# Kernel optimization log

Hardware: AMD Instinct MI355X
Metric: run time of the kernel (lower is better)

Reference implementation:

```python
import jax, jax.numpy as jnp
import numpy as np

KERNEL_MUL = 2.0
KERNEL_NUM = 5


def _mmd(source, target):
    n_s = source.shape[0]
    total = jnp.concatenate([source, target], axis=0)  # (2N, D)
    n = total.shape[0]
    # pairwise squared L2 via a^2 + b^2 - 2ab (avoids (2N,2N,D) intermediate)
    sq = jnp.sum(total * total, axis=1)  # (2N,)
    L2 = sq[:, None] + sq[None, :] - 2.0 * (total @ total.T)  # (2N, 2N)
    # torch uses L2_distance.data for bandwidth -> stop_gradient
    bandwidth = jax.lax.stop_gradient(jnp.sum(L2)) / (n * n - n)
    bandwidth = bandwidth / (KERNEL_MUL ** (KERNEL_NUM // 2))
    # multi-bandwidth RBF sum
    kernels = jnp.zeros_like(L2)
    for i in range(KERNEL_NUM):
        kernels = kernels + jnp.exp(-L2 / (bandwidth * KERNEL_MUL ** i))
    XX = kernels[:n_s, :n_s]
    YY = kernels[n_s:, n_s:]
    XY = kernels[:n_s, n_s:]
    YX = kernels[n_s:, :n_s]
    return jnp.mean(XX) + jnp.mean(YY) - jnp.mean(XY) - jnp.mean(YX)


def setup_inputs() -> dict:
    key = jax.random.key(0)
    k1, k2 = jax.random.split(key)
    source = jax.random.normal(k1, (4096, 256), dtype=jnp.float32)
    target = jax.random.normal(k2, (4096, 256), dtype=jnp.float32) + 0.5
    return {"source": source, "target": target}


def reference(source, target):
    return _mmd(source, target)
```

## Files before the change

### kernel.cpp

```cpp
#include <hip/hip_runtime.h>

typedef short bf16x8 __attribute__((ext_vector_type(8)));
typedef float f32x4 __attribute__((ext_vector_type(4)));

#define KDIM 256
#define BT 128
#define SBLK 256


__device__ __forceinline__ unsigned short f2bf(float f) {
  unsigned u = __float_as_uint(f);
  unsigned r = (u + 0x7fffu + ((u >> 16) & 1u)) >> 16;
  return (unsigned short)r;
}
__device__ __forceinline__ float bf2f(unsigned short b) {
  return __uint_as_float(((unsigned)b) << 16);
}

__device__ __forceinline__ float2 pk_add(float2 a, float2 b) {
  return make_float2(a.x + b.x, a.y + b.y);
}
__device__ __forceinline__ float2 pk_mul(float2 a, float2 b) {
  return make_float2(a.x * b.x, a.y * b.y);
}
__device__ __forceinline__ float2 pk_fma(float2 a, float2 b, float2 c) {
  return make_float2(__builtin_fmaf(a.x, b.x, c.x),
                     __builtin_fmaf(a.y, b.y, c.y));
}

__global__ __launch_bounds__(256) void mmd_stage(
    const float* __restrict__ src, const float* __restrict__ tgt, int ns,
    unsigned short* __restrict__ Tp, float* __restrict__ sq,
    float* __restrict__ pscol, float* __restrict__ psums) {
  __shared__ float sp[256];
  __shared__ float rw[4];
  int t = threadIdx.x;
  int lane = t & 63, wave = t >> 6;
  sp[t] = 0.f;
  __syncthreads();
  int sub = t & 31;
  int rsel = t >> 5;
  int ks = sub >> 2, kq = sub & 3;
  float colacc[8];
#pragma unroll
  for (int j = 0; j < 8; ++j) colacc[j] = 0.f;
  float tsq = 0.f;
#pragma unroll
  for (int it = 0; it < 4; ++it) {
    int r = blockIdx.x * 32 + it * 8 + rsel;
    const float* rp = (r < ns) ? (src + (size_t)r * KDIM)
                               : (tgt + (size_t)(r - ns) * KDIM);
    float4 v0 = *(const float4*)(rp + sub * 8);
    float4 v1 = *(const float4*)(rp + sub * 8 + 4);
    float vals[8] = {v0.x, v0.y, v0.z, v0.w, v1.x, v1.y, v1.z, v1.w};
    unsigned pk[4];
    float ssp = 0.f;
#pragma unroll
    for (int j = 0; j < 4; ++j) {
      unsigned short b0 = f2bf(vals[2 * j]);
      unsigned short b1 = f2bf(vals[2 * j + 1]);
      float x0 = bf2f(b0), x1 = bf2f(b1);
      pk[j] = (unsigned)b0 | ((unsigned)b1 << 16);
      ssp += x0 * x0 + x1 * x1;
      colacc[2 * j] += x0;
      colacc[2 * j + 1] += x1;
    }
    size_t poff = (size_t)(r >> 4) * 4096 + ks * 512 + kq * 128 + (r & 15) * 8;
    *(uint4*)(Tp + poff) = make_uint4(pk[0], pk[1], pk[2], pk[3]);
    tsq += ssp;
    float ss = ssp;
#pragma unroll
    for (int off = 16; off; off >>= 1) ss += __shfl_down(ss, off, 32);
    if (sub == 0) sq[r] = ss;
  }
#pragma unroll
  for (int j = 0; j < 8; ++j) atomicAdd(&sp[sub * 8 + j], colacc[j]);
#pragma unroll
  for (int off = 32; off; off >>= 1) tsq += __shfl_down(tsq, off, 64);
  if (lane == 0) rw[wave] = tsq;
  __syncthreads();
  pscol[(size_t)blockIdx.x * 256 + t] = sp[t];
  if (t == 0) psums[blockIdx.x] = rw[0] + rw[1] + rw[2] + rw[3];
}

__global__ __launch_bounds__(256) void mmd_prep2(
    const float* __restrict__ pscol, const float* __restrict__ psums,
    float* __restrict__ coef, float* __restrict__ out, int n) {
  __shared__ float redP[4], redS[4];
  int t = threadIdx.x;
  int lane = t & 63, wave = t >> 6;
  float cs = 0.f;
#pragma unroll 8
  for (int b = 0; b < SBLK; ++b) cs += pscol[(size_t)b * 256 + t];
  float p = cs * cs;
  float s = psums[t];
#pragma unroll
  for (int off = 32; off; off >>= 1) {
    p += __shfl_down(p, off, 64);
    s += __shfl_down(s, off, 64);
  }
  if (lane == 0) { redP[wave] = p; redS[wave] = s; }
  __syncthreads();
  if (t == 0) {
    double ssq = (double)(redP[0] + redP[1] + redP[2] + redP[3]);
    double S = (double)(redS[0] + redS[1] + redS[2] + redS[3]);
    double nn = (double)n;
    double sumL2 = 2.0 * nn * S - 2.0 * ssq;
    double bw = sumL2 / (nn * nn - nn) / 4.0;
    coef[0] = (float)(-1.4426950408889634 / (16.0 * bw));
    out[0] = 0.f;
  }
}

__global__ __launch_bounds__(256) void mmd_main(
    const unsigned short* __restrict__ Tp, const float* __restrict__ sq,
    const float* __restrict__ coef, float* __restrict__ out, int halfTiles,
    float inv) {
  __shared__ float sqa[BT];
  __shared__ float sqb[BT];
  __shared__ float red[4];

  int id = blockIdx.x;
  int bi = (int)((sqrtf(8.f * (float)id + 1.f) - 1.f) * 0.5f);
  while ((bi + 1) * (bi + 2) / 2 <= id) ++bi;
  while (bi * (bi + 1) / 2 > id) --bi;
  int bj = id - bi * (bi + 1) / 2;
  int rowBase = bi * BT, colBase = bj * BT;

  int t = threadIdx.x;
  int lane = t & 63, wave = t >> 6;

  if (t < 128) sqa[t] = sq[rowBase + t];
  else sqb[t - 128] = sq[colBase + (t - 128)];
  __syncthreads();

  int wrow = (wave >> 1) * 64, wcol = (wave & 1) * 64;

  const unsigned short* aB[4];
  const unsigned short* bB[4];
#pragma unroll
  for (int mt = 0; mt < 4; ++mt)
    aB[mt] = Tp + (size_t)(bi * 8 + (wrow >> 4) + mt) * 4096 + lane * 8;
#pragma unroll
  for (int nt = 0; nt < 4; ++nt)
    bB[nt] = Tp + (size_t)(bj * 8 + (wcol >> 4) + nt) * 4096 + lane * 8;

  f32x4 acc[4][4];
#pragma unroll
  for (int a = 0; a < 4; ++a)
#pragma unroll
    for (int b = 0; b < 4; ++b) {
      f32x4 z = {0.f, 0.f, 0.f, 0.f};
      acc[a][b] = z;
    }

#pragma unroll
  for (int ks = 0; ks < 8; ++ks) {
    bf16x8 af[4], bfv[4];
#pragma unroll
    for (int mt = 0; mt < 4; ++mt)
      af[mt] = *(const bf16x8*)(aB[mt] + ks * 512);
#pragma unroll
    for (int nt = 0; nt < 4; ++nt)
      bfv[nt] = *(const bf16x8*)(bB[nt] + ks * 512);
#pragma unroll
    for (int mt = 0; mt < 4; ++mt)
#pragma unroll
      for (int nt = 0; nt < 4; ++nt)
        acc[mt][nt] = __builtin_amdgcn_mfma_f32_16x16x32_bf16(
            af[mt], bfv[nt], acc[mt][nt], 0, 0, 0);
  }

  float c4 = coef[0];
  float m2c4 = -2.f * c4;
  float2 m2v = make_float2(m2c4, m2c4);
  int ccol = lane & 15;
  int rb = (lane >> 4) * 4;
  float ra[16];
#pragma unroll
  for (int mt = 0; mt < 4; ++mt)
#pragma unroll
    for (int rg = 0; rg < 4; ++rg)
      ra[mt * 4 + rg] = sqa[wrow + mt * 16 + rb + rg] * c4;
  float cbv[4];
#pragma unroll
  for (int nt = 0; nt < 4; ++nt) cbv[nt] = sqb[wcol + nt * 16 + ccol] * c4;

  float2 lsum2 = make_float2(0.f, 0.f);
#pragma unroll
  for (int mt = 0; mt < 4; ++mt) {
#pragma unroll
    for (int nt = 0; nt < 4; ++nt) {
      float cb = cbv[nt];
#pragma unroll
      for (int rp = 0; rp < 4; rp += 2) {
        float2 g = make_float2(acc[mt][nt][rp], acc[mt][nt][rp + 1]);
        float2 sab =
            make_float2(ra[mt * 4 + rp] + cb, ra[mt * 4 + rp + 1] + cb);
        float2 u = pk_fma(g, m2v, sab);
        float2 e = make_float2(__builtin_amdgcn_exp2f(u.x),
                               __builtin_amdgcn_exp2f(u.y));
        float2 e2 = pk_mul(e, e);
        float2 e4 = pk_mul(e2, e2);
        float2 e8 = pk_mul(e4, e4);
        float2 s = pk_add(e, e2);
        s = pk_add(s, e4);
        s = pk_add(s, e8);
        s = pk_fma(e8, e8, s);
        lsum2 = pk_add(lsum2, s);
      }
    }
  }
  float lsum = lsum2.x + lsum2.y;
#pragma unroll
  for (int off = 32; off; off >>= 1) lsum += __shfl_down(lsum, off, 64);
  if (lane == 0) red[wave] = lsum;
  __syncthreads();
  if (t == 0) {
    float w = ((bi < halfTiles) == (bj < halfTiles)) ? 1.f : -1.f;
    float f = (bi == bj) ? 1.f : 2.f;
    atomicAdd(out, w * f * inv * (red[0] + red[1] + red[2] + red[3]));
  }
}

extern "C" void kernel_launch(void* const* d_in, const int* in_sizes, int n_in,
                              void* d_out, int out_size, void* d_ws,
                              size_t ws_size, hipStream_t stream) {
  const float* src = (const float*)d_in[0];
  const float* tgt = (const float*)d_in[1];
  int ns = in_sizes[0] / KDIM;
  int ntr = in_sizes[1] / KDIM;
  int n = ns + ntr;

  char* ws = (char*)d_ws;
  unsigned short* Tp = (unsigned short*)ws;
  size_t off = (size_t)n * KDIM * sizeof(unsigned short);
  float* sq = (float*)(ws + off);    off += (size_t)n * 4;
  float* pscol = (float*)(ws + off); off += (size_t)SBLK * 256 * 4;
  float* psums = (float*)(ws + off); off += SBLK * 4;
  float* coef = (float*)(ws + off);

  float* out = (float*)d_out;
  int nb = n / BT;
  int nTiles = nb * (nb + 1) / 2;

  mmd_stage<<<SBLK, 256, 0, stream>>>(src, tgt, ns, Tp, sq, pscol, psums);
  mmd_prep2<<<1, 256, 0, stream>>>(pscol, psums, coef, out, n);
  mmd_main<<<nTiles, 256, 0, stream>>>(Tp, sq, coef, out, ns / BT,
                                       1.f / ((float)ns * (float)ns));
}
```

Before: 114.1 us.

## Make main MMD kernel persistent with grid-stride tile loop and register-side reduction

The main kernel now launches a fixed grid of 768 blocks that loop over triangular tiles with a grid stride, instead of one block per tile. Row norms are read straight from global memory into registers rather than staged through shared memory with a barrier, and per-tile weighted sums are accumulated in registers so each block does a single reduction and atomic at the end. This cuts the number of atomics, barriers and block launches, but tile count (2080) over 768 blocks leaves uneven work per block and gives up overlap between independent blocks.

```diff
diff --git a/kernel.cpp b/kernel.cpp
--- a/kernel.cpp
+++ b/kernel.cpp
@@ -6,6 +6,7 @@
 #define KDIM 256
 #define BT 128
 #define SBLK 256
+#define PBLK 768
 
 
 __device__ __forceinline__ unsigned short f2bf(float f) {
@@ -115,112 +116,107 @@
 __global__ __launch_bounds__(256) void mmd_main(
     const unsigned short* __restrict__ Tp, const float* __restrict__ sq,
     const float* __restrict__ coef, float* __restrict__ out, int halfTiles,
-    float inv) {
-  __shared__ float sqa[BT];
-  __shared__ float sqb[BT];
+    float inv, int nTiles) {
   __shared__ float red[4];
-
-  int id = blockIdx.x;
-  int bi = (int)((sqrtf(8.f * (float)id + 1.f) - 1.f) * 0.5f);
-  while ((bi + 1) * (bi + 2) / 2 <= id) ++bi;
-  while (bi * (bi + 1) / 2 > id) --bi;
-  int bj = id - bi * (bi + 1) / 2;
-  int rowBase = bi * BT, colBase = bj * BT;
-
   int t = threadIdx.x;
   int lane = t & 63, wave = t >> 6;
-
-  if (t < 128) sqa[t] = sq[rowBase + t];
-  else sqb[t - 128] = sq[colBase + (t - 128)];
-  __syncthreads();
-
   int wrow = (wave >> 1) * 64, wcol = (wave & 1) * 64;
-
-  const unsigned short* aB[4];
-  const unsigned short* bB[4];
-#pragma unroll
-  for (int mt = 0; mt < 4; ++mt)
-    aB[mt] = Tp + (size_t)(bi * 8 + (wrow >> 4) + mt) * 4096 + lane * 8;
-#pragma unroll
-  for (int nt = 0; nt < 4; ++nt)
-    bB[nt] = Tp + (size_t)(bj * 8 + (wcol >> 4) + nt) * 4096 + lane * 8;
-
-  f32x4 acc[4][4];
-#pragma unroll
-  for (int a = 0; a < 4; ++a)
-#pragma unroll
-    for (int b = 0; b < 4; ++b) {
-      f32x4 z = {0.f, 0.f, 0.f, 0.f};
-      acc[a][b] = z;
-    }
-
-#pragma unroll
-  for (int ks = 0; ks < 8; ++ks) {
-    bf16x8 af[4], bfv[4];
-#pragma unroll
-    for (int mt = 0; mt < 4; ++mt)
-      af[mt] = *(const bf16x8*)(aB[mt] + ks * 512);
-#pragma unroll
-    for (int nt = 0; nt < 4; ++nt)
-      bfv[nt] = *(const bf16x8*)(bB[nt] + ks * 512);
-#pragma unroll
-    for (int mt = 0; mt < 4; ++mt)
-#pragma unroll
-      for (int nt = 0; nt < 4; ++nt)
-        acc[mt][nt] = __builtin_amdgcn_mfma_f32_16x16x32_bf16(
-            af[mt], bfv[nt], acc[mt][nt], 0, 0, 0);
-  }
+  int ccol = lane & 15;
+  int rb = (lane >> 4) * 4;
 
   float c4 = coef[0];
   float m2c4 = -2.f * c4;
   float2 m2v = make_float2(m2c4, m2c4);
-  int ccol = lane & 15;
-  int rb = (lane >> 4) * 4;
-  float ra[16];
-#pragma unroll
-  for (int mt = 0; mt < 4; ++mt)
-#pragma unroll
-    for (int rg = 0; rg < 4; ++rg)
-      ra[mt * 4 + rg] = sqa[wrow + mt * 16 + rb + rg] * c4;
-  float cbv[4];
-#pragma unroll
-  for (int nt = 0; nt < 4; ++nt) cbv[nt] = sqb[wcol + nt * 16 + ccol] * c4;
-
-  float2 lsum2 = make_float2(0.f, 0.f);
-#pragma unroll
-  for (int mt = 0; mt < 4; ++mt) {
-#pragma unroll
-    for (int nt = 0; nt < 4; ++nt) {
-      float cb = cbv[nt];
-#pragma unroll
-      for (int rp = 0; rp < 4; rp += 2) {
-        float2 g = make_float2(acc[mt][nt][rp], acc[mt][nt][rp + 1]);
-        float2 sab =
-            make_float2(ra[mt * 4 + rp] + cb, ra[mt * 4 + rp + 1] + cb);
-        float2 u = pk_fma(g, m2v, sab);
-        float2 e = make_float2(__builtin_amdgcn_exp2f(u.x),
-                               __builtin_amdgcn_exp2f(u.y));
-        float2 e2 = pk_mul(e, e);
-        float2 e4 = pk_mul(e2, e2);
-        float2 e8 = pk_mul(e4, e4);
-        float2 s = pk_add(e, e2);
-        s = pk_add(s, e4);
-        s = pk_add(s, e8);
-        s = pk_fma(e8, e8, s);
-        lsum2 = pk_add(lsum2, s);
+  float wsum = 0.f;
+
+  for (int id = blockIdx.x; id < nTiles; id += gridDim.x) {
+    int bi = (int)((sqrtf(8.f * (float)id + 1.f) - 1.f) * 0.5f);
+    while ((bi + 1) * (bi + 2) / 2 <= id) ++bi;
+    while (bi * (bi + 1) / 2 > id) --bi;
+    int bj = id - bi * (bi + 1) / 2;
+
+    float sra[16];
+#pragma unroll
+    for (int mt = 0; mt < 4; ++mt)
+#pragma unroll
+      for (int rg = 0; rg < 4; ++rg)
+        sra[mt * 4 + rg] = sq[bi * BT + wrow + mt * 16 + rb + rg];
+    float scb[4];
+#pragma unroll
+    for (int nt = 0; nt < 4; ++nt)
+      scb[nt] = sq[bj * BT + wcol + nt * 16 + ccol];
+
+    const unsigned short* aB[4];
+    const unsigned short* bB[4];
+#pragma unroll
+    for (int mt = 0; mt < 4; ++mt)
+      aB[mt] = Tp + (size_t)(bi * 8 + (wrow >> 4) + mt) * 4096 + lane * 8;
+#pragma unroll
+    for (int nt = 0; nt < 4; ++nt)
+      bB[nt] = Tp + (size_t)(bj * 8 + (wcol >> 4) + nt) * 4096 + lane * 8;
+
+    f32x4 acc[4][4];
+#pragma unroll
+    for (int a = 0; a < 4; ++a)
+#pragma unroll
+      for (int b = 0; b < 4; ++b) {
+        f32x4 z = {0.f, 0.f, 0.f, 0.f};
+        acc[a][b] = z;
+      }
+
+#pragma unroll
+    for (int ks = 0; ks < 8; ++ks) {
+      bf16x8 af[4], bfv[4];
+#pragma unroll
+      for (int mt = 0; mt < 4; ++mt)
+        af[mt] = *(const bf16x8*)(aB[mt] + ks * 512);
+#pragma unroll
+      for (int nt = 0; nt < 4; ++nt)
+        bfv[nt] = *(const bf16x8*)(bB[nt] + ks * 512);
+#pragma unroll
+      for (int mt = 0; mt < 4; ++mt)
+#pragma unroll
+        for (int nt = 0; nt < 4; ++nt)
+          acc[mt][nt] = __builtin_amdgcn_mfma_f32_16x16x32_bf16(
+              af[mt], bfv[nt], acc[mt][nt], 0, 0, 0);
+    }
+
+    float2 lsum2 = make_float2(0.f, 0.f);
+#pragma unroll
+    for (int mt = 0; mt < 4; ++mt) {
+#pragma unroll
+      for (int nt = 0; nt < 4; ++nt) {
+        float cb = scb[nt] * c4;
+#pragma unroll
+        for (int rp = 0; rp < 4; rp += 2) {
+          float2 g = make_float2(acc[mt][nt][rp], acc[mt][nt][rp + 1]);
+          float2 sab = make_float2(
+              __builtin_fmaf(sra[mt * 4 + rp], c4, cb),
+              __builtin_fmaf(sra[mt * 4 + rp + 1], c4, cb));
+          float2 u = pk_fma(g, m2v, sab);
+          float2 e = make_float2(__builtin_amdgcn_exp2f(u.x),
+                                 __builtin_amdgcn_exp2f(u.y));
+          float2 e2 = pk_mul(e, e);
+          float2 e4 = pk_mul(e2, e2);
+          float2 e8 = pk_mul(e4, e4);
+          float2 s = pk_add(e, e2);
+          s = pk_add(s, e4);
+          s = pk_add(s, e8);
+          s = pk_fma(e8, e8, s);
+          lsum2 = pk_add(lsum2, s);
+        }
       }
     }
-  }
-  float lsum = lsum2.x + lsum2.y;
-#pragma unroll
-  for (int off = 32; off; off >>= 1) lsum += __shfl_down(lsum, off, 64);
-  if (lane == 0) red[wave] = lsum;
-  __syncthreads();
-  if (t == 0) {
-    float w = ((bi < halfTiles) == (bj < halfTiles)) ? 1.f : -1.f;
-    float f = (bi == bj) ? 1.f : 2.f;
-    atomicAdd(out, w * f * inv * (red[0] + red[1] + red[2] + red[3]));
-  }
+    float wgt = (((bi < halfTiles) == (bj < halfTiles)) ? 1.f : -1.f) *
+                ((bi == bj) ? 1.f : 2.f);
+    wsum = __builtin_fmaf(wgt, lsum2.x + lsum2.y, wsum);
+  }
+
+#pragma unroll
+  for (int off = 32; off; off >>= 1) wsum += __shfl_down(wsum, off, 64);
+  if (lane == 0) red[wave] = wsum;
+  __syncthreads();
+  if (t == 0) atomicAdd(out, inv * (red[0] + red[1] + red[2] + red[3]));
 }
 
 extern "C" void kernel_launch(void* const* d_in, const int* in_sizes, int n_in,
@@ -246,6 +242,6 @@
 
   mmd_stage<<<SBLK, 256, 0, stream>>>(src, tgt, ns, Tp, sq, pscol, psums);
   mmd_prep2<<<1, 256, 0, stream>>>(pscol, psums, coef, out, n);
-  mmd_main<<<nTiles, 256, 0, stream>>>(Tp, sq, coef, out, ns / BT,
-                                       1.f / ((float)ns * (float)ns));
-}
+  mmd_main<<<PBLK, 256, 0, stream>>>(Tp, sq, coef, out, ns / BT,
+                                     1.f / ((float)ns * (float)ns), nTiles);
+}
```

Result: no change. 113.2 us (-0.8%).
